# Kernel optimization log

Hardware: AMD Instinct MI355X
Metric: run time of the kernel (lower is better)

Reference implementation:

```python
import jax, jax.numpy as jnp
import numpy as np

A1, A2 = 16, 16            # block tile sizes (arr_size1, arr_size2)
G = 1000                   # graph_size (max node index + 1)
EG = 16000                 # number of graph edges (avg degree 16)
SIZE1 = G * A1             # input feature length  (16000)
SIZE2 = G * A2             # output feature length (16000)
NNZ = EG * A1 * A2         # expanded COO entries  (4,096,000)
B = 32                     # batch


def _expand_indices(t0, t1, a1, a2):
    """Vectorized adjust_indices: edge (t0,t1) -> tile of (row,col) pairs.
    row = t0*a2 + j, col = t1*a1 + i  for all i in [a1), j in [a2)."""
    e = t0.shape[0]
    j = np.arange(a2)
    i = np.arange(a1)
    rows = np.broadcast_to(t0[:, None, None] * a2 + j[None, None, :], (e, a1, a2)).reshape(-1)
    cols = np.broadcast_to(t1[:, None, None] * a1 + i[None, :, None], (e, a1, a2)).reshape(-1)
    return rows.astype(np.int32), cols.astype(np.int32)


def setup_inputs() -> dict:
    key = jax.random.key(0)
    ks = jax.random.split(key, 6)
    rng = np.random.default_rng(0)
    t0 = rng.integers(0, G, EG)
    t1 = rng.integers(0, G, EG)
    rows_np, cols_np = _expand_indices(t0, t1, A1, A2)
    # original init: uniform(-1/len(indices), 1/len(indices)) with len([2,nnz])==2 -> U(-0.5, 0.5)
    return {
        "x": jax.random.normal(ks[0], (B, SIZE1, 1), dtype=jnp.float32),
        "weight_mean": jax.random.uniform(ks[1], (NNZ,), jnp.float32, -0.5, 0.5),
        "weight_log_var": jnp.zeros((NNZ,), jnp.float32),
        "b_mean": jax.random.uniform(ks[2], (SIZE2,), jnp.float32, -0.5, 0.5),
        "b_log_var": jnp.zeros((SIZE2,), jnp.float32),
        "eps_w": jax.random.normal(ks[3], (NNZ,), dtype=jnp.float32),
        "eps_b": jax.random.normal(ks[4], (SIZE2,), dtype=jnp.float32),
        "rows": jnp.asarray(rows_np),
        "cols": jnp.asarray(cols_np),
    }


def reference(x, weight_mean, weight_log_var, b_mean, b_log_var, eps_w, eps_b, rows, cols):
    # reparameterization sample of sparse weight values
    values = eps_w * jnp.exp(weight_log_var) + weight_mean          # [NNZ]
    # COO spmm: out[b, r, k] += values[e] * x[b, c, k] for each (r, c) = (rows[e], cols[e])
    contrib = values[None, :, None] * x[:, cols, :]                 # [B, NNZ, 1]
    out = jnp.zeros((x.shape[0], SIZE2, x.shape[2]), x.dtype).at[:, rows, :].add(contrib)
    # reparameterized bias, broadcast over batch
    b = eps_b * jnp.exp(b_log_var) + b_mean                         # [SIZE2]
    out = out + b[None, :, None]
    # kl is explicitly zeroed in the source right before return
    return (out, jnp.asarray(0.0, dtype=x.dtype))
```

## Files before the change

kernel.cpp:

```cpp
#include <hip/hip_runtime.h>

#define EG   16000
#define NG   1000
#define BB   32
#define SIZE 16000


__global__ void count_kernel(const int* __restrict__ rows, int* __restrict__ cnt) {
    int e = blockIdx.x * blockDim.x + threadIdx.x;
    if (e < EG) {
        int t0 = rows[e << 8] >> 4;
        atomicAdd(&cnt[t0], 1);
    }
}

__global__ void scan_kernel(const int* __restrict__ cnt,
                            int* __restrict__ bin_start,
                            int* __restrict__ cursor) {
    __shared__ int s[1024];
    int t = threadIdx.x;
    int c = (t < NG) ? cnt[t] : 0;
    s[t] = c;
    __syncthreads();
    for (int off = 1; off < 1024; off <<= 1) {
        int v = (t >= off) ? s[t - off] : 0;
        __syncthreads();
        s[t] += v;
        __syncthreads();
    }
    int incl = s[t];
    if (t < NG) { bin_start[t] = incl - c; cursor[t] = incl - c; }
    if (t == 1023) bin_start[NG] = incl;
}

__global__ void scatter_kernel(const int* __restrict__ rows,
                               int* __restrict__ cursor,
                               int* __restrict__ edge_of) {
    int e = blockIdx.x * blockDim.x + threadIdx.x;
    if (e < EG) {
        int t0 = rows[e << 8] >> 4;
        int pos = atomicAdd(&cursor[t0], 1);
        edge_of[pos] = e;
    }
}


__global__ __launch_bounds__(256) void spmm_kernel(
    const float* __restrict__ wm, const float* __restrict__ wlv,
    const float* __restrict__ ew, const float* __restrict__ x,
    const float* __restrict__ bm, const float* __restrict__ blv,
    const float* __restrict__ eb, const int* __restrict__ cols,
    const int* __restrict__ edge_of, const int* __restrict__ bin_start,
    float* __restrict__ out)
{
    __shared__ float vt[256];
    __shared__ float xs[512];

    int g   = blockIdx.x;
    int tid = threadIdx.x;
    int j   = tid & 15;
    int b0  = tid >> 4;

    float acc0 = 0.f, acc1 = 0.f;
    int start = bin_start[g], end = bin_start[g + 1];

    for (int p = start; p < end; ++p) {
        int e    = edge_of[p];
        int base = e << 8;
        int t1   = cols[base] >> 4;
        vt[tid] = ew[base + tid] * __expf(wlv[base + tid]) + wm[base + tid];
        int xb = t1 << 4;
        xs[tid]       = x[ b0        * SIZE + xb + j];
        xs[tid + 256] = x[(b0 + 16)  * SIZE + xb + j];
        __syncthreads();
        #pragma unroll
        for (int i = 0; i < 16; ++i) {
            float vv = vt[(i << 4) + j];
            acc0 += vv * xs[((b0)      << 4) + i];
            acc1 += vv * xs[((b0 + 16) << 4) + i];
        }
        __syncthreads();
    }

    int r = (g << 4) + j;
    float bias = eb[r] * __expf(blv[r]) + bm[r];
    out[ b0       * SIZE + r] = acc0 + bias;
    out[(b0 + 16) * SIZE + r] = acc1 + bias;
    if (g == 0 && tid == 0) out[BB * SIZE] = 0.0f;
}

extern "C" void kernel_launch(void* const* d_in, const int* in_sizes, int n_in,
                              void* d_out, int out_size, void* d_ws, size_t ws_size,
                              hipStream_t stream) {
    const float* x   = (const float*)d_in[0];
    const float* wm  = (const float*)d_in[1];
    const float* wlv = (const float*)d_in[2];
    const float* bm  = (const float*)d_in[3];
    const float* blv = (const float*)d_in[4];
    const float* ew  = (const float*)d_in[5];
    const float* eb  = (const float*)d_in[6];
    const int* rows  = (const int*)d_in[7];
    const int* cols  = (const int*)d_in[8];
    float* out = (float*)d_out;

    char* ws = (char*)d_ws;
    int* cnt       = (int*)(ws);
    int* bin_start = (int*)(ws + 4096);
    int* cursor    = (int*)(ws + 8192);
    int* edge_of   = (int*)(ws + 12288);

    hipMemsetAsync(cnt, 0, 4096, stream);
    count_kernel<<<(EG + 255) / 256, 256, 0, stream>>>(rows, cnt);
    scan_kernel<<<1, 1024, 0, stream>>>(cnt, bin_start, cursor);
    scatter_kernel<<<(EG + 255) / 256, 256, 0, stream>>>(rows, cursor, edge_of);
    spmm_kernel<<<NG, 256, 0, stream>>>(wm, wlv, ew, x, bm, blv, eb, cols,
                                        edge_of, bin_start, out);
}
```

Baseline: 155.5 us.

## Replace row-binned gather SpMM with per-edge blocks using atomic accumulation

Drops the count/scan/scatter binning pipeline and the per-row serial loop. Instead, one block per edge computes its 16x16 tile contribution and accumulates it into the output with float atomics, after a separate kernel initializes the output with the bias. This removes four small launches and the load imbalance from rows with many edges, and exposes far more parallelism. In exchange it adds 512 atomic adds per edge, and the summation order becomes nondeterministic.

```diff
diff --git a/kernel.cpp b/kernel.cpp
--- a/kernel.cpp
+++ b/kernel.cpp
@@ -1,92 +1,59 @@
 #include <hip/hip_runtime.h>
 
 #define EG   16000
-#define NG   1000
 #define BB   32
 #define SIZE 16000
 
-
-__global__ void count_kernel(const int* __restrict__ rows, int* __restrict__ cnt) {
-    int e = blockIdx.x * blockDim.x + threadIdx.x;
-    if (e < EG) {
-        int t0 = rows[e << 8] >> 4;
-        atomicAdd(&cnt[t0], 1);
+__global__ __launch_bounds__(256) void init_out_kernel(
+    const float* __restrict__ bm, const float* __restrict__ blv,
+    const float* __restrict__ eb, float* __restrict__ out)
+{
+    int r = blockIdx.x * 256 + threadIdx.x;
+    int b = blockIdx.y;
+    if (r < SIZE) {
+        float bias = eb[r] * __expf(blv[r]) + bm[r];
+        out[b * SIZE + r] = bias;
     }
+    if (blockIdx.x == 0 && blockIdx.y == 0 && threadIdx.x == 0)
+        out[BB * SIZE] = 0.0f;
 }
 
-__global__ void scan_kernel(const int* __restrict__ cnt,
-                            int* __restrict__ bin_start,
-                            int* __restrict__ cursor) {
-    __shared__ int s[1024];
-    int t = threadIdx.x;
-    int c = (t < NG) ? cnt[t] : 0;
-    s[t] = c;
-    __syncthreads();
-    for (int off = 1; off < 1024; off <<= 1) {
-        int v = (t >= off) ? s[t - off] : 0;
-        __syncthreads();
-        s[t] += v;
-        __syncthreads();
-    }
-    int incl = s[t];
-    if (t < NG) { bin_start[t] = incl - c; cursor[t] = incl - c; }
-    if (t == 1023) bin_start[NG] = incl;
-}
-
-__global__ void scatter_kernel(const int* __restrict__ rows,
-                               int* __restrict__ cursor,
-                               int* __restrict__ edge_of) {
-    int e = blockIdx.x * blockDim.x + threadIdx.x;
-    if (e < EG) {
-        int t0 = rows[e << 8] >> 4;
-        int pos = atomicAdd(&cursor[t0], 1);
-        edge_of[pos] = e;
-    }
-}
-
-
-__global__ __launch_bounds__(256) void spmm_kernel(
+__global__ __launch_bounds__(256) void edge_kernel(
     const float* __restrict__ wm, const float* __restrict__ wlv,
     const float* __restrict__ ew, const float* __restrict__ x,
-    const float* __restrict__ bm, const float* __restrict__ blv,
-    const float* __restrict__ eb, const int* __restrict__ cols,
-    const int* __restrict__ edge_of, const int* __restrict__ bin_start,
+    const int* __restrict__ rows, const int* __restrict__ cols,
     float* __restrict__ out)
 {
     __shared__ float vt[256];
     __shared__ float xs[512];
 
-    int g   = blockIdx.x;
-    int tid = threadIdx.x;
-    int j   = tid & 15;
-    int b0  = tid >> 4;
+    int e    = blockIdx.x;
+    int tid  = threadIdx.x;
+    int base = e << 8;
+
+    int t0 = rows[base] >> 4;
+    int t1 = cols[base] >> 4;
+
+    vt[tid] = ew[base + tid] * __expf(wlv[base + tid]) + wm[base + tid];
+
+    int j  = tid & 15;
+    int b0 = tid >> 4;
+    int xb = t1 << 4;
+    xs[tid]       = x[ b0        * SIZE + xb + j];
+    xs[tid + 256] = x[(b0 + 16)  * SIZE + xb + j];
+    __syncthreads();
 
     float acc0 = 0.f, acc1 = 0.f;
-    int start = bin_start[g], end = bin_start[g + 1];
-
-    for (int p = start; p < end; ++p) {
-        int e    = edge_of[p];
-        int base = e << 8;
-        int t1   = cols[base] >> 4;
-        vt[tid] = ew[base + tid] * __expf(wlv[base + tid]) + wm[base + tid];
-        int xb = t1 << 4;
-        xs[tid]       = x[ b0        * SIZE + xb + j];
-        xs[tid + 256] = x[(b0 + 16)  * SIZE + xb + j];
-        __syncthreads();
-        #pragma unroll
-        for (int i = 0; i < 16; ++i) {
-            float vv = vt[(i << 4) + j];
-            acc0 += vv * xs[((b0)      << 4) + i];
-            acc1 += vv * xs[((b0 + 16) << 4) + i];
-        }
-        __syncthreads();
+    #pragma unroll
+    for (int i = 0; i < 16; ++i) {
+        float vv = vt[(i << 4) + j];
+        acc0 += vv * xs[((b0)      << 4) + i];
+        acc1 += vv * xs[((b0 + 16) << 4) + i];
     }
 
-    int r = (g << 4) + j;
-    float bias = eb[r] * __expf(blv[r]) + bm[r];
-    out[ b0       * SIZE + r] = acc0 + bias;
-    out[(b0 + 16) * SIZE + r] = acc1 + bias;
-    if (g == 0 && tid == 0) out[BB * SIZE] = 0.0f;
+    int r = (t0 << 4) + j;
+    unsafeAtomicAdd(&out[ b0       * SIZE + r], acc0);
+    unsafeAtomicAdd(&out[(b0 + 16) * SIZE + r], acc1);
 }
 
 extern "C" void kernel_launch(void* const* d_in, const int* in_sizes, int n_in,
@@ -103,16 +70,6 @@
     const int* cols  = (const int*)d_in[8];
     float* out = (float*)d_out;
 
-    char* ws = (char*)d_ws;
-    int* cnt       = (int*)(ws);
-    int* bin_start = (int*)(ws + 4096);
-    int* cursor    = (int*)(ws + 8192);
-    int* edge_of   = (int*)(ws + 12288);
-
-    hipMemsetAsync(cnt, 0, 4096, stream);
-    count_kernel<<<(EG + 255) / 256, 256, 0, stream>>>(rows, cnt);
-    scan_kernel<<<1, 1024, 0, stream>>>(cnt, bin_start, cursor);
-    scatter_kernel<<<(EG + 255) / 256, 256, 0, stream>>>(rows, cursor, edge_of);
-    spmm_kernel<<<NG, 256, 0, stream>>>(wm, wlv, ew, x, bm, blv, eb, cols,
-                                        edge_of, bin_start, out);
+    init_out_kernel<<<dim3((SIZE + 255) / 256, BB), 256, 0, stream>>>(bm, blv, eb, out);
+    edge_kernel<<<EG, 256, 0, stream>>>(wm, wlv, ew, x, rows, cols, out);
 }
```

Result: faster. 137.0 us (-11.9%).

## Double-buffer edge tiles, process two edges per step with vectorized loads

Applied to the files above, without the earlier changes.

Rewrites the spmm kernel so each iteration handles two edges at once. Half the threads load weight tiles with float4 loads and the other half load x slices, and the next pair's global loads are prefetched into registers while the current pair is computed from a double-buffered shared tile. Each thread now accumulates a 4-wide output strip, and the two edge halves are reduced through shared memory at the end, followed by a float4 bias add and store. This targets the per-edge global-load latency and the two syncs per edge, at the cost of more registers and an extra reduction step.

```diff
diff --git a/kernel.cpp b/kernel.cpp
--- a/kernel.cpp
+++ b/kernel.cpp
@@ -5,6 +5,7 @@
 #define BB   32
 #define SIZE 16000
 
+typedef float f32x4 __attribute__((ext_vector_type(4)));
 
 __global__ void count_kernel(const int* __restrict__ rows, int* __restrict__ cnt) {
     int e = blockIdx.x * blockDim.x + threadIdx.x;
@@ -44,7 +45,6 @@
     }
 }
 
-
 __global__ __launch_bounds__(256) void spmm_kernel(
     const float* __restrict__ wm, const float* __restrict__ wlv,
     const float* __restrict__ ew, const float* __restrict__ x,
@@ -53,40 +53,124 @@
     const int* __restrict__ edge_of, const int* __restrict__ bin_start,
     float* __restrict__ out)
 {
-    __shared__ float vt[256];
-    __shared__ float xs[512];
+    __shared__ f32x4 vt[2][2][64];
+    __shared__ f32x4 xs[2][2][128];
 
     int g   = blockIdx.x;
     int tid = threadIdx.x;
-    int j   = tid & 15;
-    int b0  = tid >> 4;
-
-    float acc0 = 0.f, acc1 = 0.f;
     int start = bin_start[g], end = bin_start[g + 1];
-
-    for (int p = start; p < end; ++p) {
-        int e    = edge_of[p];
-        int base = e << 8;
-        int t1   = cols[base] >> 4;
-        vt[tid] = ew[base + tid] * __expf(wlv[base + tid]) + wm[base + tid];
-        int xb = t1 << 4;
-        xs[tid]       = x[ b0        * SIZE + xb + j];
-        xs[tid + 256] = x[(b0 + 16)  * SIZE + xb + j];
-        __syncthreads();
+    int n  = end - start;
+    int np = (n + 1) >> 1;
+
+    int cs = tid >> 7;
+    int jg = tid & 3;
+    int cb = (tid >> 2) & 31;
+    float acc0 = 0.f, acc1 = 0.f, acc2 = 0.f, acc3 = 0.f;
+
+    bool wrole = (tid < 128);
+    int  ss = wrole ? (tid >> 6) : ((tid - 128) >> 6);
+    int  sc = tid & 63;
+
+    int eA = -1, eB = -1, t1A = 0, t1B = 0;
+    int eA2 = -1, eB2 = -1, t1A2 = 0, t1B2 = 0;
+
+    auto load_idx = [&](int q, int& ea, int& ebv, int& ta, int& tb) {
+        int i0 = start + (q << 1);
+        ea  = (i0     < end) ? edge_of[i0]     : -1;
+        ebv = (i0 + 1 < end) ? edge_of[i0 + 1] : -1;
+        ta  = (ea  >= 0) ? (cols[(long)ea  << 8] >> 4) : 0;
+        tb  = (ebv >= 0) ? (cols[(long)ebv << 8] >> 4) : 0;
+    };
+
+    f32x4 m4, l4, g4;
+    f32x4 xv0, xv1;
+    bool  sval = false;
+
+    auto stage_issue = [&](int ea, int ebv, int ta, int tb) {
+        int e  = ss ? ebv : ea;
+        int t1 = ss ? tb  : ta;
+        sval = (e >= 0);
+        if (wrole) {
+            long q = ((long)(sval ? e : 0) << 6) + sc;
+            m4 = ((const f32x4*)wm)[q];
+            l4 = ((const f32x4*)wlv)[q];
+            g4 = ((const f32x4*)ew)[q];
+        } else {
+            const f32x4* x4 = (const f32x4*)x;
+            int xrow = t1 << 2;
+            xv0 = x4[(sc >> 2)        * (SIZE / 4) + xrow + (sc & 3)];
+            int c1 = sc + 64;
+            xv1 = x4[(c1 >> 2)        * (SIZE / 4) + xrow + (c1 & 3)];
+        }
+    };
+
+    auto stage_write = [&](int buf) {
+        if (wrole) {
+            f32x4 v = {0.f, 0.f, 0.f, 0.f};
+            if (sval) {
+                v.x = g4.x * __expf(l4.x) + m4.x;
+                v.y = g4.y * __expf(l4.y) + m4.y;
+                v.z = g4.z * __expf(l4.z) + m4.z;
+                v.w = g4.w * __expf(l4.w) + m4.w;
+            }
+            vt[buf][ss][sc] = v;
+        } else {
+            xs[buf][ss][sc]      = xv0;
+            xs[buf][ss][sc + 64] = xv1;
+        }
+    };
+
+    auto compute = [&](int buf) {
+        f32x4 x0 = xs[buf][cs][(cb << 2) + 0];
+        f32x4 x1 = xs[buf][cs][(cb << 2) + 1];
+        f32x4 x2 = xs[buf][cs][(cb << 2) + 2];
+        f32x4 x3 = xs[buf][cs][(cb << 2) + 3];
+        float xr[16] = { x0.x, x0.y, x0.z, x0.w,  x1.x, x1.y, x1.z, x1.w,
+                         x2.x, x2.y, x2.z, x2.w,  x3.x, x3.y, x3.z, x3.w };
         #pragma unroll
         for (int i = 0; i < 16; ++i) {
-            float vv = vt[(i << 4) + j];
-            acc0 += vv * xs[((b0)      << 4) + i];
-            acc1 += vv * xs[((b0 + 16) << 4) + i];
-        }
+            f32x4 w = vt[buf][cs][(i << 2) + jg];
+            float xi = xr[i];
+            acc0 += w.x * xi; acc1 += w.y * xi; acc2 += w.z * xi; acc3 += w.w * xi;
+        }
+    };
+
+    load_idx(0, eA, eB, t1A, t1B);
+    stage_issue(eA, eB, t1A, t1B);
+    load_idx(1, eA2, eB2, t1A2, t1B2);
+    stage_write(0);
+    __syncthreads();
+
+    for (int p = 0; p < np; ++p) {
+        bool more = (p + 1 < np);
+        if (more) {
+            stage_issue(eA2, eB2, t1A2, t1B2);
+            load_idx(p + 2, eA2, eB2, t1A2, t1B2);
+        }
+        compute(p & 1);
+        if (more) stage_write((p + 1) & 1);
         __syncthreads();
     }
 
-    int r = (g << 4) + j;
-    float bias = eb[r] * __expf(blv[r]) + bm[r];
-    out[ b0       * SIZE + r] = acc0 + bias;
-    out[(b0 + 16) * SIZE + r] = acc1 + bias;
-    if (g == 0 && tid == 0) out[BB * SIZE] = 0.0f;
+    f32x4* sred = &xs[0][0][0];
+    int lane128 = tid & 127;
+    if (cs == 1) sred[lane128] = f32x4{acc0, acc1, acc2, acc3};
+    __syncthreads();
+    if (cs == 0) {
+        f32x4 o = sred[lane128];
+        acc0 += o.x; acc1 += o.y; acc2 += o.z; acc3 += o.w;
+        int r0 = (g << 4) + (jg << 2);
+        f32x4 b4 = *(const f32x4*)&bm[r0];
+        f32x4 v4 = *(const f32x4*)&blv[r0];
+        f32x4 e4 = *(const f32x4*)&eb[r0];
+        f32x4 o4;
+        o4.x = acc0 + (e4.x * __expf(v4.x) + b4.x);
+        o4.y = acc1 + (e4.y * __expf(v4.y) + b4.y);
+        o4.z = acc2 + (e4.z * __expf(v4.z) + b4.z);
+        o4.w = acc3 + (e4.w * __expf(v4.w) + b4.w);
+        *(f32x4*)&out[cb * SIZE + r0] = o4;
+    }
+    if (g == 0 && tid == 0) out[(long)BB * SIZE] = 0.0f;
 }
 
 extern "C" void kernel_launch(void* const* d_in, const int* in_sizes, int n_in,
```

Result: slower. 158.9 us (+2.2%).
